# Optimization experiments

Measured on AMD Instinct MI355X. Metric: run time of the kernel, lower is better.

The kernel has to match this reference:

```python
import jax, jax.numpy as jnp
import numpy as np

N_NODES = 100000
N_EDGES = 1600000
N_GRAPHS = 256
DIMS = [128, 128, 128, 128]  # gcn_layers_dim -> 3 GCNConv layers


def setup_inputs() -> dict:
    key = jax.random.key(0)
    ks = jax.random.split(key, 12)
    inp = {
        "x": jax.random.normal(ks[0], (N_NODES, DIMS[0]), jnp.float32),
        "edge_index": jax.random.randint(ks[1], (2, N_EDGES), 0, N_NODES),
        "edge_weight": jax.random.uniform(ks[2], (N_EDGES,), jnp.float32),
        "batch": jnp.sort(jax.random.randint(ks[3], (N_NODES,), 0, N_GRAPHS)),
    }
    for i in range(3):
        fan_in = DIMS[i]
        scale = 1.0 / np.sqrt(fan_in)
        inp[f"W{i+1}"] = jax.random.uniform(ks[4 + 2 * i], (DIMS[i], DIMS[i + 1]),
                                             jnp.float32, -scale, scale)
        inp[f"b{i+1}"] = jax.random.uniform(ks[5 + 2 * i], (DIMS[i + 1],),
                                             jnp.float32, -scale, scale)
    return inp


def reference(x, edge_index, edge_weight, batch, W1, b1, W2, b2, W3, b3):
    n = x.shape[0]
    # PyG GCNConv: add self-loops with weight 1, symmetric normalization.
    loop = jnp.arange(n)
    row = jnp.concatenate([edge_index[0], loop])  # source nodes
    col = jnp.concatenate([edge_index[1], loop])  # target nodes (aggregation index)
    w = jnp.concatenate([edge_weight, jnp.ones((n,), x.dtype)])
    deg = jax.ops.segment_sum(w, col, num_segments=n)
    dinv = jnp.where(deg > 0, jax.lax.rsqrt(deg), jnp.zeros_like(deg))
    norm = dinv[row] * w * dinv[col]  # [E+N]

    # global_mean_pool setup
    counts = jax.ops.segment_sum(jnp.ones((n,), x.dtype), batch,
                                 num_segments=N_GRAPHS)
    counts = jnp.maximum(counts, 1.0)[:, None]

    def gcn_conv(h, W, b):
        hl = h @ W                      # linear projection first (PyG order)
        msg = hl[row] * norm[:, None]   # gather + edge scaling
        out = jax.ops.segment_sum(msg, col, num_segments=n)  # scatter-add
        return out + b

    embeddings = []
    h = x
    for W, b in ((W1, b1), (W2, b2), (W3, b3)):
        h = gcn_conv(h, W, b)
        h = jax.nn.relu(h)              # relu_layers_index = [0,1,2]
        emb = jax.ops.segment_sum(h, batch, num_segments=N_GRAPHS) / counts
        embeddings.append(emb)          # gep = global_mean_pool
    return tuple(embeddings)
```

## Files before the change

### kernel.cpp

```cpp
#include <hip/hip_runtime.h>


typedef short short8 __attribute__((ext_vector_type(8)));
typedef float f32x4  __attribute__((ext_vector_type(4)));

__device__ inline unsigned pack_bf16x2(float a, float b) {
    unsigned ua = __float_as_uint(a);
    ua = (ua + 0x7FFFu + ((ua >> 16) & 1u)) >> 16;
    unsigned ub = __float_as_uint(b);
    ub = (ub + 0x7FFFu + ((ub >> 16) & 1u)) >> 16;
    return ua | (ub << 16);
}
__device__ inline ushort bf16_1(float a) {
    unsigned ua = __float_as_uint(a);
    return (ushort)((ua + 0x7FFFu + ((ua >> 16) & 1u)) >> 16);
}
__device__ inline float bf_lo(unsigned u) { return __uint_as_float(u << 16); }
__device__ inline float bf_hi(unsigned u) { return __uint_as_float(u & 0xFFFF0000u); }


template <bool F32IN>
__device__ __forceinline__ void gemm_tile(const void* __restrict__ Hin,
                                          const ushort* __restrict__ WbT,
                                          unsigned* __restrict__ O, int M,
                                          int bid, unsigned* sOut) {
    int lane = threadIdx.x & 63;
    int wv = threadIdx.x >> 6;
    int quad = lane >> 4;
    int mrow = lane & 15;
    int m0 = bid * 128 + wv * 32;
    int r0 = m0 + mrow;
    int r1 = r0 + 16;
    int r0c = r0 < M ? r0 : M - 1;
    int r1c = r1 < M ? r1 : M - 1;

    short8 a0[4], a1[4];
    if (F32IN) {
        const float* Hf = (const float*)Hin;
#pragma unroll
        for (int s = 0; s < 4; s++) {
            const float4* p0 = (const float4*)(Hf + (size_t)r0c * 128 + s * 32 + quad * 8);
            const float4* p1 = (const float4*)(Hf + (size_t)r1c * 128 + s * 32 + quad * 8);
            float4 f0 = p0[0], f1 = p0[1];
            float4 g0 = p1[0], g1 = p1[1];
            union { short8 s8; unsigned u[4]; } t0, t1;
            t0.u[0] = pack_bf16x2(f0.x, f0.y); t0.u[1] = pack_bf16x2(f0.z, f0.w);
            t0.u[2] = pack_bf16x2(f1.x, f1.y); t0.u[3] = pack_bf16x2(f1.z, f1.w);
            t1.u[0] = pack_bf16x2(g0.x, g0.y); t1.u[1] = pack_bf16x2(g0.z, g0.w);
            t1.u[2] = pack_bf16x2(g1.x, g1.y); t1.u[3] = pack_bf16x2(g1.z, g1.w);
            a0[s] = t0.s8; a1[s] = t1.s8;
        }
    } else {
        const unsigned* Hb = (const unsigned*)Hin;
#pragma unroll
        for (int s = 0; s < 4; s++) {
            a0[s] = *(const short8*)(Hb + (size_t)r0c * 64 + s * 16 + quad * 4);
            a1[s] = *(const short8*)(Hb + (size_t)r1c * 64 + s * 16 + quad * 4);
        }
    }
    f32x4 acc0[8], acc1[8];
#pragma unroll
    for (int t = 0; t < 8; t++) {
        acc0[t] = (f32x4){0.f, 0.f, 0.f, 0.f};
        acc1[t] = (f32x4){0.f, 0.f, 0.f, 0.f};
    }
#pragma unroll
    for (int s = 0; s < 4; s++) {
#pragma unroll
        for (int t = 0; t < 8; t++) {
            short8 b = *(const short8*)(WbT + (t * 16 + mrow) * 128 + s * 32 + quad * 8);
            acc0[t] = __builtin_amdgcn_mfma_f32_16x16x32_bf16(a0[s], b, acc0[t], 0, 0, 0);
            acc1[t] = __builtin_amdgcn_mfma_f32_16x16x32_bf16(a1[s], b, acc1[t], 0, 0, 0);
        }
    }
    ushort* so = (ushort*)(sOut + wv * 32 * 64);
#pragma unroll
    for (int t = 0; t < 8; t++) {
#pragma unroll
        for (int r = 0; r < 4; r++) {
            int lr = quad * 4 + r;
            int c = t * 16 + mrow;
            so[lr * 128 + c] = bf16_1(acc0[t][r]);
            so[(lr + 16) * 128 + c] = bf16_1(acc1[t][r]);
        }
    }
    __syncthreads();
    const unsigned* si = sOut + wv * 32 * 64;
#pragma unroll 8
    for (int r = 0; r < 32; r++) {
        int row = m0 + r;
        if (row < M) O[(size_t)row * 64 + lane] = si[r * 64 + lane];
    }
}

__device__ __forceinline__ void pool_tile(const unsigned* __restrict__ HB,
                                          const int* __restrict__ gb,
                                          float* __restrict__ outp, int g,
                                          float* part) {
    int lane = threadIdx.x & 63, w = threadIdx.x >> 6;
    int s = gb[g], e = gb[g + 1];
    float ax = 0.f, ay = 0.f;
    for (int i = s + w; i < e; i += 4) {
        unsigned u = HB[(size_t)i * 64 + lane];
        ax += bf_lo(u); ay += bf_hi(u);
    }
    part[w * 128 + lane * 2] = ax;
    part[w * 128 + lane * 2 + 1] = ay;
    __syncthreads();
    if (threadIdx.x < 128) {
        float sum = part[threadIdx.x] + part[128 + threadIdx.x]
                  + part[256 + threadIdx.x] + part[384 + threadIdx.x];
        float c = (float)(e - s);
        outp[g * 128 + threadIdx.x] = sum / fmaxf(c, 1.0f);
    }
}


__global__ void k_prep(const int* __restrict__ batch, int* __restrict__ gb,
                       int G, int N,
                       const float* __restrict__ W0, const float* __restrict__ W1,
                       const float* __restrict__ W2, ushort* __restrict__ WbT) {
    int id = blockIdx.x * blockDim.x + threadIdx.x;
    if (id <= G) {
        int lo = 0, hi = N;
        while (lo < hi) { int mid = (lo + hi) >> 1; if (batch[mid] < id) lo = mid + 1; else hi = mid; }
        gb[id] = lo;
    }
    if (id < 3 * 16384) {
        int l = id >> 14;
        const float* W = (l == 0) ? W0 : ((l == 1) ? W1 : W2);
        int id2 = id & 16383;
        int n = id2 & 127, k = id2 >> 7;
        WbT[l * 16384 + n * 128 + k] = bf16_1(W[k * 128 + n]);
    }
}

__global__ __launch_bounds__(256) void k_phase1(const int* __restrict__ ei,
                                                int* __restrict__ hist, int E,
                                                const float* __restrict__ x,
                                                const ushort* __restrict__ WbT,
                                                unsigned* __restrict__ O, int M,
                                                int nbGemm, int nbCount) {
    __shared__ unsigned sBuf[8192];
    if (blockIdx.x < nbGemm) {
        gemm_tile<true>(x, WbT, O, M, blockIdx.x, sBuf);
        return;
    }
    int blk = blockIdx.x - nbGemm;
    unsigned* hcnt = sBuf;
    int t = threadIdx.x;
    for (int i = t; i < nbGemm; i += 256) hcnt[i] = 0;
    __syncthreads();
    int base = blk * 8192;
    for (int i = t; i < 8192; i += 256) {
        int e = base + i;
        if (e < E) atomicAdd(&hcnt[(unsigned)ei[E + e] >> 7], 1u);
    }
    __syncthreads();
    for (int b = t; b < nbGemm; b += 256)
        hist[b * nbCount + blk] = (int)hcnt[b];
}

__global__ __launch_bounds__(1024) void k_scan1(const int* __restrict__ cnt,
                                                int* __restrict__ pre,
                                                int* __restrict__ bsum, int n) {
    __shared__ int wsum[16];
    int t = threadIdx.x, lane = t & 63, w = t >> 6;
    int i = blockIdx.x * 1024 + t;
    int v = (i < n) ? cnt[i] : 0;
    int x = v;
#pragma unroll
    for (int off = 1; off < 64; off <<= 1) {
        int y = __shfl_up(x, off, 64);
        if (lane >= off) x += y;
    }
    if (lane == 63) wsum[w] = x;
    __syncthreads();
    int woff = 0, tot = 0;
#pragma unroll
    for (int q = 0; q < 16; q++) { int s = wsum[q]; if (q < w) woff += s; tot += s; }
    if (i < n) pre[i] = woff + x - v;
    if (t == 0) bsum[blockIdx.x] = tot;
}

__global__ __launch_bounds__(256) void k_scat(const int* __restrict__ ei,
                                              const float* __restrict__ ew,
                                              const int* __restrict__ pre,
                                              const int* __restrict__ bsumRaw,
                                              int* __restrict__ bucketStart,
                                              int2* __restrict__ recs,
                                              int E, int nbkt, int nbCount,
                                              int nbScan) {
    __shared__ int sRaw[256];
    __shared__ int sPre[256];
    __shared__ int sWt[4];
    __shared__ int sBase[784];
    __shared__ unsigned rk[784];
    int t = threadIdx.x;
    sRaw[t] = (t < nbScan) ? bsumRaw[t] : 0;
    for (int b = t; b < nbkt; b += 256) rk[b] = 0;
    __syncthreads();
    int lane = t & 63, w2 = t >> 6;
    int v = sRaw[t];
    int x = v;
#pragma unroll
    for (int off = 1; off < 64; off <<= 1) {
        int y = __shfl_up(x, off, 64);
        if (lane >= off) x += y;
    }
    if (lane == 63) sWt[w2] = x;
    __syncthreads();
    int base = 0;
#pragma unroll
    for (int q = 0; q < 4; q++) { if (q < w2) base += sWt[q]; }
    sPre[t] = base + x - v;
    __syncthreads();
    int blk = blockIdx.x;
    for (int b = t; b < nbkt; b += 256) {
        int f = b * nbCount + blk;
        sBase[b] = pre[f] + sPre[f >> 10];
    }
    if (blk == 0) {
        for (int b = t; b <= nbkt; b += 256) {
            if (b == nbkt) bucketStart[b] = E;
            else { int f = b * nbCount; bucketStart[b] = pre[f] + sPre[f >> 10]; }
        }
    }
    __syncthreads();
    int e0 = blk * 8192;
    for (int i = t; i < 8192; i += 256) {
        int e = e0 + i;
        if (e < E) {
            int r = ei[e];
            int c = ei[E + e];
            float w = ew[e];
            int b = (unsigned)c >> 7;
            unsigned rank = atomicAdd(&rk[b], 1u);
            int2 rec; rec.x = r | ((c & 127) << 17); rec.y = __float_as_int(w);
            recs[sBase[b] + (int)rank] = rec;
        }
    }
}

__global__ __launch_bounds__(256) void k_fin(const int2* __restrict__ recs,
                                             const int* __restrict__ bucketStart,
                                             int2* __restrict__ csr,
                                             int* __restrict__ ptrv,
                                             float* __restrict__ dinv,
                                             int N, int nbkt) {
    __shared__ unsigned scnt[128];
    __shared__ float swdeg[128];
    __shared__ float sdinv[128];
    __shared__ unsigned sTot0;
    int t = threadIdx.x;
    int b = blockIdx.x;
    int e0 = bucketStart[b], e1 = bucketStart[b + 1];
    int FB = e0 + b * 128;
    if (t < 128) { scnt[t] = 0u; swdeg[t] = 0.f; }
    __syncthreads();
    for (int i = e0 + t; i < e1; i += 256) {
        int2 rec = recs[i];
        int cl = (rec.x >> 17) & 127;
        atomicAdd(&scnt[cl], 1u);
        atomicAdd(&swdeg[cl], __int_as_float(rec.y));
    }
    __syncthreads();
    unsigned myc = (t < 128) ? scnt[t] : 0u;
    int lane = t & 63, wv = t >> 6;
    unsigned inc = myc;
#pragma unroll
    for (int off = 1; off < 64; off <<= 1) {
        unsigned y = __shfl_up(inc, off, 64);
        if (lane >= off) inc += y;
    }
    if (t == 63) sTot0 = inc;
    __syncthreads();
    unsigned excl = inc - myc + ((wv == 1) ? sTot0 : 0u);
    if (t < 128) {
        float dv = rsqrtf(1.0f + swdeg[t]);
        sdinv[t] = dv;
        scnt[t] = excl + (unsigned)t + 1u;
        int node = b * 128 + t;
        int start = FB + (int)excl + t;
        if (node < N) {
            ptrv[node] = start;
            dinv[node] = dv;
            int2 sv; sv.x = node; sv.y = __float_as_int(dv);
            csr[start] = sv;
        }
    }
    if (b == nbkt - 1 && t == 0) ptrv[N] = e1 + N;
    __syncthreads();
    for (int i = e0 + t; i < e1; i += 256) {
        int2 rec = recs[i];
        int cl = (rec.x >> 17) & 127;
        int r = rec.x & 131071;
        unsigned rank = atomicAdd(&scnt[cl], 1u);
        float y = __int_as_float(rec.y) * sdinv[cl];
        int2 mv; mv.x = r; mv.y = __float_as_int(y);
        csr[FB + (int)rank] = mv;
    }
}

__global__ __launch_bounds__(256) void k_norm2(int2* __restrict__ csr,
                                               const float* __restrict__ dinv,
                                               int E) {
    int base = blockIdx.x * 1024 + threadIdx.x;
#pragma unroll
    for (int q = 0; q < 4; q++) {
        int e = base + q * 256;
        if (e < E) {
            int2 m = csr[e];
            m.y = __float_as_int(__int_as_float(m.y) * dinv[m.x]);
            csr[e] = m;
        }
    }
}

__global__ __launch_bounds__(256) void k_agg(const unsigned* __restrict__ HL,
                                             const int* __restrict__ ptr,
                                             const int2* __restrict__ csr,
                                             const float* __restrict__ bias,
                                             unsigned* __restrict__ Hout, int M) {
    __shared__ int2 sM[4 * 64];
    int node = (int)((blockIdx.x * blockDim.x + threadIdx.x) >> 6);
    if (node >= M) return;
    int lane = threadIdx.x & 63;
    int half = lane >> 5;
    int q = lane & 31;
    int2* mbase = &sM[(threadIdx.x >> 6) * 64];
    int e0 = ptr[node], e1 = ptr[node + 1];
    int deg = e1 - e0;
    int nbv = deg < 64 ? deg : 64;
    if (lane < nbv) mbase[lane] = csr[e0 + lane];
    const uint2* HL2 = (const uint2*)HL;
    float a0 = 0.f, a1 = 0.f, a2 = 0.f, a3 = 0.f;
    int j = half;
    for (; j + 16 <= nbv; j += 16) {
        int2 m[8]; uint2 u[8];
#pragma unroll
        for (int t = 0; t < 8; t++) m[t] = mbase[j + 2 * t];
#pragma unroll
        for (int t = 0; t < 8; t++) u[t] = HL2[(size_t)m[t].x * 32 + q];
#pragma unroll
        for (int t = 0; t < 8; t++) {
            float nv = __int_as_float(m[t].y);
            a0 += nv * bf_lo(u[t].x); a1 += nv * bf_hi(u[t].x);
            a2 += nv * bf_lo(u[t].y); a3 += nv * bf_hi(u[t].y);
        }
    }
    for (; j + 8 <= nbv; j += 8) {
        int2 m[4]; uint2 u[4];
#pragma unroll
        for (int t = 0; t < 4; t++) m[t] = mbase[j + 2 * t];
#pragma unroll
        for (int t = 0; t < 4; t++) u[t] = HL2[(size_t)m[t].x * 32 + q];
#pragma unroll
        for (int t = 0; t < 4; t++) {
            float nv = __int_as_float(m[t].y);
            a0 += nv * bf_lo(u[t].x); a1 += nv * bf_hi(u[t].x);
            a2 += nv * bf_lo(u[t].y); a3 += nv * bf_hi(u[t].y);
        }
    }
    for (; j < nbv; j += 2) {
        int2 m = mbase[j];
        uint2 u = HL2[(size_t)m.x * 32 + q];
        float nv = __int_as_float(m.y);
        a0 += nv * bf_lo(u.x); a1 += nv * bf_hi(u.x);
        a2 += nv * bf_lo(u.y); a3 += nv * bf_hi(u.y);
    }
    for (int e = e0 + 64 + half; e < e1; e += 2) {
        int2 m = csr[e];
        uint2 u = HL2[(size_t)m.x * 32 + q];
        float nv = __int_as_float(m.y);
        a0 += nv * bf_lo(u.x); a1 += nv * bf_hi(u.x);
        a2 += nv * bf_lo(u.y); a3 += nv * bf_hi(u.y);
    }
    a0 += __shfl_xor(a0, 32, 64);
    a1 += __shfl_xor(a1, 32, 64);
    a2 += __shfl_xor(a2, 32, 64);
    a3 += __shfl_xor(a3, 32, 64);
    float4 bv = ((const float4*)bias)[q];
    float r0 = fmaxf(a0 + bv.x, 0.f);
    float r1 = fmaxf(a1 + bv.y, 0.f);
    float r2 = fmaxf(a2 + bv.z, 0.f);
    float r3 = fmaxf(a3 + bv.w, 0.f);
    if (half == 0) {
        uint2 pv;
        pv.x = pack_bf16x2(r0, r1);
        pv.y = pack_bf16x2(r2, r3);
        ((uint2*)(Hout + (size_t)node * 64))[q] = pv;
    }
}

__global__ __launch_bounds__(256) void k_gemm_pool(const unsigned* __restrict__ Hb,
                                                   const ushort* __restrict__ WbT,
                                                   unsigned* __restrict__ O, int M,
                                                   const int* __restrict__ gb,
                                                   float* __restrict__ outp,
                                                   int nbGemm) {
    __shared__ unsigned sBuf[8192];
    if (blockIdx.x < nbGemm) {
        gemm_tile<false>(Hb, WbT, O, M, blockIdx.x, sBuf);
        return;
    }
    pool_tile(Hb, gb, outp, blockIdx.x - nbGemm, (float*)sBuf);
}

extern "C" void kernel_launch(void* const* d_in, const int* in_sizes, int n_in,
                              void* d_out, int out_size, void* d_ws, size_t ws_size,
                              hipStream_t stream) {
    const float* x     = (const float*)d_in[0];
    const int*   ei    = (const int*)d_in[1];
    const float* ew    = (const float*)d_in[2];
    const int*   batch = (const int*)d_in[3];
    const float* Wt[3] = {(const float*)d_in[4], (const float*)d_in[6], (const float*)d_in[8]};
    const float* bt[3] = {(const float*)d_in[5], (const float*)d_in[7], (const float*)d_in[9]};
    float* out = (float*)d_out;

    const int D = 128;
    const int N = in_sizes[0] / D;
    const int E = in_sizes[2];
    const int G = out_size / (3 * D);

    char* p = (char*)d_ws;
    auto alloc = [&](size_t bytes) {
        void* r = (void*)p;
        p += (bytes + 255) & ~(size_t)255;
        return r;
    };
    int nbkt    = (N + 127) / 128;
    int nbCount = (E + 8191) / 8192;
    int F       = nbkt * nbCount;
    int nbScan  = (F + 1023) / 1024;

    int*      ptr    = (int*)alloc((size_t)(N + 1) * 4);
    int*      bsum   = (int*)alloc((size_t)256 * 4);
    int*      gb     = (int*)alloc((size_t)(G + 1) * 4);
    int*      bstart = (int*)alloc((size_t)(nbkt + 1) * 4);
    float*    dinv   = (float*)alloc((size_t)N * 4);
    ushort*   WbT    = (ushort*)alloc((size_t)3 * 16384 * 2);
    int2*     csr    = (int2*)alloc((size_t)(E + N) * 8);
    unsigned* bufHL  = (unsigned*)alloc((size_t)N * 64 * 4);
    unsigned* bufH   = (unsigned*)alloc((size_t)N * 64 * 4);
    int*  hist = (int*)csr;
    int*  pre  = hist + F;
    int2* recs = (int2*)bufH;

    int nbGemm = (N + 127) / 128;
    int prepWork = 3 * 16384;

    k_prep<<<(prepWork + 255) / 256, 256, 0, stream>>>(batch, gb, G, N,
                                                       Wt[0], Wt[1], Wt[2], WbT);
    k_phase1<<<nbGemm + nbCount, 256, 0, stream>>>(ei, hist, E, x, WbT,
                                                   bufHL, N, nbGemm, nbCount);
    k_scan1<<<nbScan, 1024, 0, stream>>>(hist, pre, bsum, F);
    k_scat<<<nbCount, 256, 0, stream>>>(ei, ew, pre, bsum, bstart, recs,
                                        E, nbkt, nbCount, nbScan);
    k_fin<<<nbkt, 256, 0, stream>>>(recs, bstart, csr, ptr, dinv, N, nbkt);
    k_norm2<<<(E + N + 1023) / 1024, 256, 0, stream>>>(csr, dinv, E + N);

    k_agg<<<(N + 3) / 4, 256, 0, stream>>>(bufHL, ptr, csr, bt[0], bufH, N);
    k_gemm_pool<<<nbGemm + G, 256, 0, stream>>>(bufH, WbT + 16384, bufHL, N,
                                                gb, out + 0 * (size_t)G * D, nbGemm);
    k_agg<<<(N + 3) / 4, 256, 0, stream>>>(bufHL, ptr, csr, bt[1], bufH, N);
    k_gemm_pool<<<nbGemm + G, 256, 0, stream>>>(bufH, WbT + 2 * 16384, bufHL, N,
                                                gb, out + 1 * (size_t)G * D, nbGemm);
    k_agg<<<(N + 3) / 4, 256, 0, stream>>>(bufHL, ptr, csr, bt[2], bufH, N);
    k_gemm_pool<<<G, 256, 0, stream>>>(bufH, WbT, nullptr, 0,
                                       gb, out + 2 * (size_t)G * D, 0);
}
```

Measured before the change: 524.4 us.

## Fuse aggregation, next-layer GEMM and mean pooling into one per-tile layer kernel

Replaces the separate aggregation kernel and the GEMM+pool kernel with one kernel per layer. Each block aggregates 128 nodes into a swizzled LDS tile, runs the next layer's MFMA projection straight from LDS, and pools partial graph sums with atomicAdd into an output zeroed in k_prep. This avoids writing and re-reading the intermediate H buffer and cuts kernel launches. In exchange, each block has only 4 waves working through 128 nodes serially, which lowers gather parallelism and latency hiding, and pooling now relies on float atomics.

```diff
diff --git a/kernel.cpp b/kernel.cpp
--- a/kernel.cpp
+++ b/kernel.cpp
@@ -18,12 +18,15 @@
 __device__ inline float bf_lo(unsigned u) { return __uint_as_float(u << 16); }
 __device__ inline float bf_hi(unsigned u) { return __uint_as_float(u & 0xFFFF0000u); }
 
-
-template <bool F32IN>
-__device__ __forceinline__ void gemm_tile(const void* __restrict__ Hin,
-                                          const ushort* __restrict__ WbT,
-                                          unsigned* __restrict__ O, int M,
-                                          int bid, unsigned* sOut) {
+__device__ inline int hswz(int row, int c) {
+    return row * 64 + ((((c >> 2) ^ (row & 15)) << 2) | (c & 3));
+}
+
+
+__device__ __forceinline__ void gemm_tile_f32(const float* __restrict__ Hf,
+                                              const ushort* __restrict__ WbT,
+                                              unsigned* __restrict__ O, int M,
+                                              int bid, unsigned* sOut) {
     int lane = threadIdx.x & 63;
     int wv = threadIdx.x >> 6;
     int quad = lane >> 4;
@@ -35,28 +38,18 @@
     int r1c = r1 < M ? r1 : M - 1;
 
     short8 a0[4], a1[4];
-    if (F32IN) {
-        const float* Hf = (const float*)Hin;
-#pragma unroll
-        for (int s = 0; s < 4; s++) {
-            const float4* p0 = (const float4*)(Hf + (size_t)r0c * 128 + s * 32 + quad * 8);
-            const float4* p1 = (const float4*)(Hf + (size_t)r1c * 128 + s * 32 + quad * 8);
-            float4 f0 = p0[0], f1 = p0[1];
-            float4 g0 = p1[0], g1 = p1[1];
-            union { short8 s8; unsigned u[4]; } t0, t1;
-            t0.u[0] = pack_bf16x2(f0.x, f0.y); t0.u[1] = pack_bf16x2(f0.z, f0.w);
-            t0.u[2] = pack_bf16x2(f1.x, f1.y); t0.u[3] = pack_bf16x2(f1.z, f1.w);
-            t1.u[0] = pack_bf16x2(g0.x, g0.y); t1.u[1] = pack_bf16x2(g0.z, g0.w);
-            t1.u[2] = pack_bf16x2(g1.x, g1.y); t1.u[3] = pack_bf16x2(g1.z, g1.w);
-            a0[s] = t0.s8; a1[s] = t1.s8;
-        }
-    } else {
-        const unsigned* Hb = (const unsigned*)Hin;
-#pragma unroll
-        for (int s = 0; s < 4; s++) {
-            a0[s] = *(const short8*)(Hb + (size_t)r0c * 64 + s * 16 + quad * 4);
-            a1[s] = *(const short8*)(Hb + (size_t)r1c * 64 + s * 16 + quad * 4);
-        }
+#pragma unroll
+    for (int s = 0; s < 4; s++) {
+        const float4* p0 = (const float4*)(Hf + (size_t)r0c * 128 + s * 32 + quad * 8);
+        const float4* p1 = (const float4*)(Hf + (size_t)r1c * 128 + s * 32 + quad * 8);
+        float4 f0 = p0[0], f1 = p0[1];
+        float4 g0 = p1[0], g1 = p1[1];
+        union { short8 s8; unsigned u[4]; } t0, t1;
+        t0.u[0] = pack_bf16x2(f0.x, f0.y); t0.u[1] = pack_bf16x2(f0.z, f0.w);
+        t0.u[2] = pack_bf16x2(f1.x, f1.y); t0.u[3] = pack_bf16x2(f1.z, f1.w);
+        t1.u[0] = pack_bf16x2(g0.x, g0.y); t1.u[1] = pack_bf16x2(g0.z, g0.w);
+        t1.u[2] = pack_bf16x2(g1.x, g1.y); t1.u[3] = pack_bf16x2(g1.z, g1.w);
+        a0[s] = t0.s8; a1[s] = t1.s8;
     }
     f32x4 acc0[8], acc1[8];
 #pragma unroll
@@ -93,34 +86,14 @@
     }
 }
 
-__device__ __forceinline__ void pool_tile(const unsigned* __restrict__ HB,
-                                          const int* __restrict__ gb,
-                                          float* __restrict__ outp, int g,
-                                          float* part) {
-    int lane = threadIdx.x & 63, w = threadIdx.x >> 6;
-    int s = gb[g], e = gb[g + 1];
-    float ax = 0.f, ay = 0.f;
-    for (int i = s + w; i < e; i += 4) {
-        unsigned u = HB[(size_t)i * 64 + lane];
-        ax += bf_lo(u); ay += bf_hi(u);
-    }
-    part[w * 128 + lane * 2] = ax;
-    part[w * 128 + lane * 2 + 1] = ay;
-    __syncthreads();
-    if (threadIdx.x < 128) {
-        float sum = part[threadIdx.x] + part[128 + threadIdx.x]
-                  + part[256 + threadIdx.x] + part[384 + threadIdx.x];
-        float c = (float)(e - s);
-        outp[g * 128 + threadIdx.x] = sum / fmaxf(c, 1.0f);
-    }
-}
-
 
 __global__ void k_prep(const int* __restrict__ batch, int* __restrict__ gb,
                        int G, int N,
                        const float* __restrict__ W0, const float* __restrict__ W1,
-                       const float* __restrict__ W2, ushort* __restrict__ WbT) {
+                       const float* __restrict__ W2, ushort* __restrict__ WbT,
+                       float* __restrict__ outv, int outN) {
     int id = blockIdx.x * blockDim.x + threadIdx.x;
+    if (id < outN) outv[id] = 0.f;
     if (id <= G) {
         int lo = 0, hi = N;
         while (lo < hi) { int mid = (lo + hi) >> 1; if (batch[mid] < id) lo = mid + 1; else hi = mid; }
@@ -143,7 +116,7 @@
                                                 int nbGemm, int nbCount) {
     __shared__ unsigned sBuf[8192];
     if (blockIdx.x < nbGemm) {
-        gemm_tile<true>(x, WbT, O, M, blockIdx.x, sBuf);
+        gemm_tile_f32(x, WbT, O, M, blockIdx.x, sBuf);
         return;
     }
     int blk = blockIdx.x - nbGemm;
@@ -317,94 +290,155 @@
     }
 }
 
-__global__ __launch_bounds__(256) void k_agg(const unsigned* __restrict__ HL,
-                                             const int* __restrict__ ptr,
-                                             const int2* __restrict__ csr,
-                                             const float* __restrict__ bias,
-                                             unsigned* __restrict__ Hout, int M) {
+template <bool HASGEMM>
+__global__ __launch_bounds__(256) void k_layer(const unsigned* __restrict__ HL,
+                                               const int* __restrict__ ptr,
+                                               const int2* __restrict__ csr,
+                                               const float* __restrict__ bias,
+                                               const int* __restrict__ gb, int G,
+                                               float* __restrict__ outp,
+                                               const ushort* __restrict__ WbT,
+                                               unsigned* __restrict__ O, int N) {
+    __shared__ unsigned hT[8192];
     __shared__ int2 sM[4 * 64];
-    int node = (int)((blockIdx.x * blockDim.x + threadIdx.x) >> 6);
-    if (node >= M) return;
-    int lane = threadIdx.x & 63;
+    int t = threadIdx.x;
+    int lane = t & 63, wv = t >> 6;
     int half = lane >> 5;
     int q = lane & 31;
-    int2* mbase = &sM[(threadIdx.x >> 6) * 64];
-    int e0 = ptr[node], e1 = ptr[node + 1];
-    int deg = e1 - e0;
-    int nbv = deg < 64 ? deg : 64;
-    if (lane < nbv) mbase[lane] = csr[e0 + lane];
+    int base = blockIdx.x * 128;
+    int2* mbase = &sM[wv * 64];
     const uint2* HL2 = (const uint2*)HL;
-    float a0 = 0.f, a1 = 0.f, a2 = 0.f, a3 = 0.f;
-    int j = half;
-    for (; j + 16 <= nbv; j += 16) {
-        int2 m[8]; uint2 u[8];
-#pragma unroll
-        for (int t = 0; t < 8; t++) m[t] = mbase[j + 2 * t];
-#pragma unroll
-        for (int t = 0; t < 8; t++) u[t] = HL2[(size_t)m[t].x * 32 + q];
-#pragma unroll
-        for (int t = 0; t < 8; t++) {
-            float nv = __int_as_float(m[t].y);
-            a0 += nv * bf_lo(u[t].x); a1 += nv * bf_hi(u[t].x);
-            a2 += nv * bf_lo(u[t].y); a3 += nv * bf_hi(u[t].y);
-        }
-    }
-    for (; j + 8 <= nbv; j += 8) {
-        int2 m[4]; uint2 u[4];
-#pragma unroll
-        for (int t = 0; t < 4; t++) m[t] = mbase[j + 2 * t];
-#pragma unroll
-        for (int t = 0; t < 4; t++) u[t] = HL2[(size_t)m[t].x * 32 + q];
-#pragma unroll
-        for (int t = 0; t < 4; t++) {
-            float nv = __int_as_float(m[t].y);
-            a0 += nv * bf_lo(u[t].x); a1 += nv * bf_hi(u[t].x);
-            a2 += nv * bf_lo(u[t].y); a3 += nv * bf_hi(u[t].y);
-        }
-    }
-    for (; j < nbv; j += 2) {
-        int2 m = mbase[j];
-        uint2 u = HL2[(size_t)m.x * 32 + q];
-        float nv = __int_as_float(m.y);
-        a0 += nv * bf_lo(u.x); a1 += nv * bf_hi(u.x);
-        a2 += nv * bf_lo(u.y); a3 += nv * bf_hi(u.y);
-    }
-    for (int e = e0 + 64 + half; e < e1; e += 2) {
-        int2 m = csr[e];
-        uint2 u = HL2[(size_t)m.x * 32 + q];
-        float nv = __int_as_float(m.y);
-        a0 += nv * bf_lo(u.x); a1 += nv * bf_hi(u.x);
-        a2 += nv * bf_lo(u.y); a3 += nv * bf_hi(u.y);
-    }
-    a0 += __shfl_xor(a0, 32, 64);
-    a1 += __shfl_xor(a1, 32, 64);
-    a2 += __shfl_xor(a2, 32, 64);
-    a3 += __shfl_xor(a3, 32, 64);
     float4 bv = ((const float4*)bias)[q];
-    float r0 = fmaxf(a0 + bv.x, 0.f);
-    float r1 = fmaxf(a1 + bv.y, 0.f);
-    float r2 = fmaxf(a2 + bv.z, 0.f);
-    float r3 = fmaxf(a3 + bv.w, 0.f);
-    if (half == 0) {
-        uint2 pv;
-        pv.x = pack_bf16x2(r0, r1);
-        pv.y = pack_bf16x2(r2, r3);
-        ((uint2*)(Hout + (size_t)node * 64))[q] = pv;
-    }
-}
-
-__global__ __launch_bounds__(256) void k_gemm_pool(const unsigned* __restrict__ Hb,
-                                                   const ushort* __restrict__ WbT,
-                                                   unsigned* __restrict__ O, int M,
-                                                   const int* __restrict__ gb,
-                                                   float* __restrict__ outp,
-                                                   int nbGemm) {
-    __shared__ unsigned sBuf[8192];
-    if (blockIdx.x < nbGemm) {
-        gemm_tile<false>(Hb, WbT, O, M, blockIdx.x, sBuf);
-        return;
-    }
-    pool_tile(Hb, gb, outp, blockIdx.x - nbGemm, (float*)sBuf);
+
+    for (int i = 0; i < 32; i++) {
+        int row = wv * 32 + i;
+        int node = base + row;
+        if (node >= N) break;
+        int e0 = ptr[node], e1 = ptr[node + 1];
+        int deg = e1 - e0;
+        int nbv = deg < 64 ? deg : 64;
+        if (lane < nbv) mbase[lane] = csr[e0 + lane];
+        float a0 = 0.f, a1 = 0.f, a2 = 0.f, a3 = 0.f;
+        int j = half;
+        for (; j + 8 <= nbv; j += 8) {
+            int2 m[4]; uint2 u[4];
+#pragma unroll
+            for (int k = 0; k < 4; k++) m[k] = mbase[j + 2 * k];
+#pragma unroll
+            for (int k = 0; k < 4; k++) u[k] = HL2[(size_t)m[k].x * 32 + q];
+#pragma unroll
+            for (int k = 0; k < 4; k++) {
+                float nv = __int_as_float(m[k].y);
+                a0 += nv * bf_lo(u[k].x); a1 += nv * bf_hi(u[k].x);
+                a2 += nv * bf_lo(u[k].y); a3 += nv * bf_hi(u[k].y);
+            }
+        }
+        for (; j < nbv; j += 2) {
+            int2 m = mbase[j];
+            uint2 u = HL2[(size_t)m.x * 32 + q];
+            float nv = __int_as_float(m.y);
+            a0 += nv * bf_lo(u.x); a1 += nv * bf_hi(u.x);
+            a2 += nv * bf_lo(u.y); a3 += nv * bf_hi(u.y);
+        }
+        for (int e = e0 + 64 + half; e < e1; e += 2) {
+            int2 m = csr[e];
+            uint2 u = HL2[(size_t)m.x * 32 + q];
+            float nv = __int_as_float(m.y);
+            a0 += nv * bf_lo(u.x); a1 += nv * bf_hi(u.x);
+            a2 += nv * bf_lo(u.y); a3 += nv * bf_hi(u.y);
+        }
+        a0 += __shfl_xor(a0, 32, 64);
+        a1 += __shfl_xor(a1, 32, 64);
+        a2 += __shfl_xor(a2, 32, 64);
+        a3 += __shfl_xor(a3, 32, 64);
+        if (half == 0) {
+            float r0 = fmaxf(a0 + bv.x, 0.f);
+            float r1 = fmaxf(a1 + bv.y, 0.f);
+            float r2 = fmaxf(a2 + bv.z, 0.f);
+            float r3 = fmaxf(a3 + bv.w, 0.f);
+            int ix = hswz(row, 2 * q);
+            hT[ix] = pack_bf16x2(r0, r1);
+            hT[ix + 1] = pack_bf16x2(r2, r3);
+        }
+    }
+    __syncthreads();
+
+    f32x4 acc0[8], acc1[8];
+    if (HASGEMM) {
+        int quad = lane >> 4;
+        int mrow = lane & 15;
+        int R0 = wv * 32 + mrow, R1 = R0 + 16;
+        short8 a0[4], a1[4];
+#pragma unroll
+        for (int s = 0; s < 4; s++) {
+            a0[s] = *(const short8*)&hT[R0 * 64 + (((s * 4 + quad) ^ (R0 & 15)) << 2)];
+            a1[s] = *(const short8*)&hT[R1 * 64 + (((s * 4 + quad) ^ (R1 & 15)) << 2)];
+        }
+#pragma unroll
+        for (int k = 0; k < 8; k++) {
+            acc0[k] = (f32x4){0.f, 0.f, 0.f, 0.f};
+            acc1[k] = (f32x4){0.f, 0.f, 0.f, 0.f};
+        }
+#pragma unroll
+        for (int s = 0; s < 4; s++) {
+#pragma unroll
+            for (int k = 0; k < 8; k++) {
+                short8 b = *(const short8*)(WbT + (k * 16 + mrow) * 128 + s * 32 + quad * 8);
+                acc0[k] = __builtin_amdgcn_mfma_f32_16x16x32_bf16(a0[s], b, acc0[k], 0, 0, 0);
+                acc1[k] = __builtin_amdgcn_mfma_f32_16x16x32_bf16(a1[s], b, acc1[k], 0, 0, 0);
+            }
+        }
+    }
+
+    if (t < 128) {
+        int f = t, c = f >> 1, ch = f & 1;
+        int glo = 0, ghi = G;
+        while (glo < ghi) {
+            int mid = (glo + ghi + 1) >> 1;
+            if (gb[mid] <= base) glo = mid; else ghi = mid - 1;
+        }
+        for (int g = glo; g < G; g++) {
+            int gs = gb[g];
+            if (gs >= base + 128) break;
+            int ge = gb[g + 1];
+            int r0 = gs > base ? gs : base;
+            int r1 = ge < base + 128 ? ge : base + 128;
+            if (r1 > N) r1 = N;
+            if (r1 <= r0) continue;
+            float s = 0.f;
+            for (int r = r0; r < r1; r++) {
+                unsigned u = hT[hswz(r - base, c)];
+                s += ch ? bf_hi(u) : bf_lo(u);
+            }
+            float cnt = (float)(ge - gs);
+            atomicAdd(&outp[g * 128 + f], s / fmaxf(cnt, 1.f));
+        }
+    }
+
+    if (HASGEMM) {
+        __syncthreads();
+        int quad = lane >> 4;
+        int mrow = lane & 15;
+        ushort* so = (ushort*)(hT + wv * 32 * 64);
+#pragma unroll
+        for (int k = 0; k < 8; k++) {
+#pragma unroll
+            for (int r = 0; r < 4; r++) {
+                int lr = quad * 4 + r;
+                int c = k * 16 + mrow;
+                so[lr * 128 + c] = bf16_1(acc0[k][r]);
+                so[(lr + 16) * 128 + c] = bf16_1(acc1[k][r]);
+            }
+        }
+        __syncthreads();
+        const unsigned* si = hT + wv * 32 * 64;
+        int m0 = base + wv * 32;
+#pragma unroll 8
+        for (int r = 0; r < 32; r++) {
+            int row = m0 + r;
+            if (row < N) O[(size_t)row * 64 + lane] = si[r * 64 + lane];
+        }
+    }
 }
 
 extern "C" void kernel_launch(void* const* d_in, const int* in_sizes, int n_in,
@@ -441,32 +475,33 @@
     float*    dinv   = (float*)alloc((size_t)N * 4);
     ushort*   WbT    = (ushort*)alloc((size_t)3 * 16384 * 2);
     int2*     csr    = (int2*)alloc((size_t)(E + N) * 8);
-    unsigned* bufHL  = (unsigned*)alloc((size_t)N * 64 * 4);
-    unsigned* bufH   = (unsigned*)alloc((size_t)N * 64 * 4);
+    unsigned* bufA   = (unsigned*)alloc((size_t)N * 64 * 4);
+    unsigned* bufB   = (unsigned*)alloc((size_t)N * 64 * 4);
     int*  hist = (int*)csr;
     int*  pre  = hist + F;
-    int2* recs = (int2*)bufH;
-
-    int nbGemm = (N + 127) / 128;
-    int prepWork = 3 * 16384;
+    int2* recs = (int2*)bufB;
+
+    int nbGemm = nbkt;
+    int prepWork = 3 * G * D;
 
     k_prep<<<(prepWork + 255) / 256, 256, 0, stream>>>(batch, gb, G, N,
-                                                       Wt[0], Wt[1], Wt[2], WbT);
+                                                       Wt[0], Wt[1], Wt[2], WbT,
+                                                       out, 3 * G * D);
     k_phase1<<<nbGemm + nbCount, 256, 0, stream>>>(ei, hist, E, x, WbT,
-                                                   bufHL, N, nbGemm, nbCount);
+                                                   bufA, N, nbGemm, nbCount);
     k_scan1<<<nbScan, 1024, 0, stream>>>(hist, pre, bsum, F);
     k_scat<<<nbCount, 256, 0, stream>>>(ei, ew, pre, bsum, bstart, recs,
                                         E, nbkt, nbCount, nbScan);
     k_fin<<<nbkt, 256, 0, stream>>>(recs, bstart, csr, ptr, dinv, N, nbkt);
     k_norm2<<<(E + N + 1023) / 1024, 256, 0, stream>>>(csr, dinv, E + N);
 
-    k_agg<<<(N + 3) / 4, 256, 0, stream>>>(bufHL, ptr, csr, bt[0], bufH, N);
-    k_gemm_pool<<<nbGemm + G, 256, 0, stream>>>(bufH, WbT + 16384, bufHL, N,
-                                                gb, out + 0 * (size_t)G * D, nbGemm);
-    k_agg<<<(N + 3) / 4, 256, 0, stream>>>(bufHL, ptr, csr, bt[1], bufH, N);
-    k_gemm_pool<<<nbGemm + G, 256, 0, stream>>>(bufH, WbT + 2 * 16384, bufHL, N,
-                                                gb, out + 1 * (size_t)G * D, nbGemm);
-    k_agg<<<(N + 3) / 4, 256, 0, stream>>>(bufHL, ptr, csr, bt[2], bufH, N);
-    k_gemm_pool<<<G, 256, 0, stream>>>(bufH, WbT, nullptr, 0,
-                                       gb, out + 2 * (size_t)G * D, 0);
-}
+    k_layer<true><<<nbkt, 256, 0, stream>>>(bufA, ptr, csr, bt[0], gb, G,
+                                            out + 0 * (size_t)G * D,
+                                            WbT + 16384, bufB, N);
+    k_layer<true><<<nbkt, 256, 0, stream>>>(bufB, ptr, csr, bt[1], gb, G,
+                                            out + 1 * (size_t)G * D,
+                                            WbT + 2 * 16384, bufA, N);
+    k_layer<false><<<nbkt, 256, 0, stream>>>(bufA, ptr, csr, bt[2], gb, G,
+                                             out + 2 * (size_t)G * D,
+                                             nullptr, nullptr, N);
+}
```

Result: slower. 689.7 us (+31.5%).
